# Performance work log

Measured on AMD Instinct MI355X. Metric: run time of the kernel, lower is better.

## Reference

```python
import jax, jax.numpy as jnp
import numpy as np

# ---- left-hand kinematic constants (from ShadowHandModule.create_left_hand_nodes_and_joints) ----
N_NODES = 29
PARENTS = [-1, 0, 1, 2, 3, 4, 5, 1, 7, 8, 9, 10, 1, 12, 13, 14, 15, 1, 17, 18, 19, 20, 21, 1, 23, 24, 25, 26, 27]
# joint index driving each node (-1 = fixed link such as fingertips)
NODE_JOINT = [0, 1, 2, 3, 4, 5, -1, 6, 7, 8, 9, -1, 10, 11, 12, 13, -1, 14, 15, 16, 17, 18, -1, 19, 20, 21, 22, 23, -1]
TRANS = np.array([
    [0.0, 0.0, 0.0], [0.0, 0.0, 0.034],
    [-0.033, 0.0, 0.095], [0.0, 0.0, 0.0], [0.0, 0.0, 0.045], [0.0, 0.0, 0.025], [0.0, 0.0, 0.026],
    [-0.011, 0.0, 0.099], [0.0, 0.0, 0.0], [0.0, 0.0, 0.045], [0.0, 0.0, 0.025], [0.0, 0.0, 0.026],
    [0.011, 0.0, 0.095], [0.0, 0.0, 0.0], [0.0, 0.0, 0.045], [0.0, 0.0, 0.025], [0.0, 0.0, 0.026],
    [0.033, 0.0, 0.02071], [0.0, 0.0, 0.06579], [0.0, 0.0, 0.0], [0.0, 0.0, 0.045], [0.0, 0.0, 0.025], [0.0, 0.0, 0.026],
    [-0.034, -0.0085, 0.029], [0.0, 0.0, 0.0], [0.0, 0.0, 0.038], [0.0, 0.0, 0.0], [0.0, 0.0, 0.032], [0.0, 0.0, 0.0275],
], dtype=np.float32)
AXES = np.array([
    [0.0, 1.0, 0.0], [1.0, 0.0, 0.0],
    [0.0, 1.0, 0.0], [1.0, 0.0, 0.0], [1.0, 0.0, 0.0], [1.0, 0.0, 0.0],
    [0.0, 1.0, 0.0], [1.0, 0.0, 0.0], [1.0, 0.0, 0.0], [1.0, 0.0, 0.0],
    [0.0, -1.0, 0.0], [1.0, 0.0, 0.0], [1.0, 0.0, 0.0], [1.0, 0.0, 0.0],
    [0.573576, 0.0, -0.819152], [0.0, -1.0, 0.0], [1.0, 0.0, 0.0], [1.0, 0.0, 0.0], [1.0, 0.0, 0.0],
    [0.0, 0.0, 1.0], [-1.0, 0.0, 0.0], [1.0, 0.0, 0.0], [0.0, -1.0, 0.0], [1.0, 0.0, 0.0],
], dtype=np.float32)
MIN_RAD = np.array([-0.523599, -0.698132, -0.349066, 0.0, 0.0, 0.0, -0.349066, 0.0, 0.0, 0.0,
                    -0.349066, 0.0, 0.0, 0.0, 0.0, -0.349066, 0.0, 0.0, 0.0,
                    -1.0472, 0.0, -0.20944, -0.698132, 0.0], dtype=np.float32)
MAX_RAD = np.array([0.174533, 0.488692, 0.349066, 1.5708, 1.5708, 1.5708, 0.349066, 1.5708, 1.5708, 1.5708,
                    0.349066, 1.5708, 1.5708, 1.5708, 0.785398, 0.349066, 1.5708, 1.5708, 1.5708,
                    1.0472, 1.22173, 0.20944, 0.698132, 1.5708], dtype=np.float32)
THBASE_QUAT = np.array([0.0, 0.382683, 0.0, -0.92388], dtype=np.float32)
THDISTAL_QUAT = np.array([0.707107, 0.0, 0.0, -0.707107], dtype=np.float32)
BATCH = 262144


def hat(v):
    x, y, z = v[..., 0], v[..., 1], v[..., 2]
    o = jnp.zeros_like(x)
    return jnp.stack([jnp.stack([o, -z, y], -1),
                      jnp.stack([z, o, -x], -1),
                      jnp.stack([-y, x, o], -1)], -2)


def rot_angle_axis(angle, axis):
    # angle [B,J], axis [J,3] -> [B,J,3,3] (Rodrigues)
    s = jnp.sin(angle)[..., None, None]
    c = jnp.cos(angle)[..., None, None]
    K = hat(axis)          # [J,3,3]
    K2 = jnp.matmul(K, K)  # [J,3,3]
    return jnp.eye(3, dtype=angle.dtype) + s * K + (1.0 - c) * K2


def rot_from_quat(q):
    w, x, y, z = q[0], q[1], q[2], q[3]
    return jnp.array([
        [1.0 - 2.0 * (y * y + z * z), 2.0 * (x * y - z * w), 2.0 * (x * z + y * w)],
        [2.0 * (x * y + z * w), 1.0 - 2.0 * (x * x + z * z), 2.0 * (y * z - x * w)],
        [2.0 * (x * z - y * w), 2.0 * (y * z + x * w), 1.0 - 2.0 * (x * x + y * y)],
    ], dtype=q.dtype)


def setup_inputs() -> dict:
    key = jax.random.key(0)
    u = jax.random.uniform(key, (BATCH, 24), dtype=jnp.float32)
    angles = jnp.asarray(MIN_RAD) + u * jnp.asarray(MAX_RAD - MIN_RAD)
    return {"angles": angles}


def reference(angles):
    # angles: [B, 24] joint angles -> node positions [B, 29, 3]
    B = angles.shape[0]
    q = jnp.clip(angles, jnp.asarray(MIN_RAD), jnp.asarray(MAX_RAD))
    Rj = rot_angle_axis(q, jnp.asarray(AXES))  # [B,24,3,3]
    fixed = {23: rot_from_quat(jnp.asarray(THBASE_QUAT)),
             27: rot_from_quat(jnp.asarray(THDISTAL_QUAT))}
    eye = jnp.broadcast_to(jnp.eye(3, dtype=angles.dtype), (B, 3, 3))
    Rg = [None] * N_NODES
    tg = [None] * N_NODES
    for i in range(N_NODES):  # fixed 29-node kinematic tree, topological order
        j = NODE_JOINT[i]
        Rl = Rj[:, j] if j >= 0 else eye
        if i in fixed:  # body quat applied before joint rotation (MJCF convention)
            Rl = jnp.einsum('ij,bjk->bik', fixed[i], Rl)
        tl = jnp.asarray(TRANS[i])
        p = PARENTS[i]
        if p < 0:
            Rg[i] = Rl
            tg[i] = jnp.broadcast_to(tl, (B, 3))
        else:
            # multiply_transform: (Rp @ Rl, Rp @ tl + tp)
            Rg[i] = jnp.einsum('bij,bjk->bik', Rg[p], Rl)
            tg[i] = jnp.einsum('bij,j->bi', Rg[p], tl) + tg[p]
    return jnp.stack(tg, axis=1)  # [B, 29, 3]
```

## Files before the change

kernel.cpp:

```cpp
#include <hip/hip_runtime.h>

namespace fk {

typedef float f32x4 __attribute__((ext_vector_type(4)));

struct V3 { float x, y, z; };
struct M3 { V3 c0, c1, c2; };

__device__ __forceinline__ V3 axpy(float a, V3 x, V3 y) {
    return V3{ fmaf(a, x.x, y.x), fmaf(a, x.y, y.y), fmaf(a, x.z, y.z) };
}
__device__ __forceinline__ V3 sc(float a, V3 x) { return V3{ a * x.x, a * x.y, a * x.z }; }

__device__ __forceinline__ M3 mulRx(const M3& R, float s, float c) {
    return M3{ R.c0,
               axpy(s,  R.c2, sc(c, R.c1)),
               axpy(-s, R.c1, sc(c, R.c2)) };
}
__device__ __forceinline__ M3 mulRy(const M3& R, float s, float c) {
    return M3{ axpy(-s, R.c2, sc(c, R.c0)),
               R.c1,
               axpy(s,  R.c0, sc(c, R.c2)) };
}

__global__ __launch_bounds__(64) void fk_kernel(const float* __restrict__ angles,
                                                float* __restrict__ out, int B) {
    __shared__ float lds[64 * 87];

    const int tid = threadIdx.x;
    const int b = blockIdx.x * 64 + tid;
    const bool valid = (b < B);

    if (valid) {
        const float4* ap = reinterpret_cast<const float4*>(angles + (size_t)b * 24);
        float q[24];
        {
            float4 v;
            v = ap[0]; q[0]=v.x;  q[1]=v.y;  q[2]=v.z;  q[3]=v.w;
            v = ap[1]; q[4]=v.x;  q[5]=v.y;  q[6]=v.z;  q[7]=v.w;
            v = ap[2]; q[8]=v.x;  q[9]=v.y;  q[10]=v.z; q[11]=v.w;
            v = ap[3]; q[12]=v.x; q[13]=v.y; q[14]=v.z; q[15]=v.w;
            v = ap[4]; q[16]=v.x; q[17]=v.y; q[18]=v.z; q[19]=v.w;
            v = ap[5]; q[20]=v.x; q[21]=v.y; q[22]=v.z; q[23]=v.w;
        }

        constexpr float MN[24] = {-0.523599f,-0.698132f,-0.349066f,0.f,0.f,0.f,-0.349066f,0.f,0.f,0.f,
                                  -0.349066f,0.f,0.f,0.f,0.f,-0.349066f,0.f,0.f,0.f,
                                  -1.0472f,0.f,-0.20944f,-0.698132f,0.f};
        constexpr float MX[24] = {0.174533f,0.488692f,0.349066f,1.5708f,1.5708f,1.5708f,0.349066f,1.5708f,1.5708f,1.5708f,
                                  0.349066f,1.5708f,1.5708f,1.5708f,0.785398f,0.349066f,1.5708f,1.5708f,1.5708f,
                                  1.0472f,1.22173f,0.20944f,0.698132f,1.5708f};
        float s[24], c[24];
        #pragma unroll
        for (int j = 0; j < 24; ++j) {
            float a = fminf(fmaxf(q[j], MN[j]), MX[j]);
            __sincosf(a, &s[j], &c[j]);
        }

        float* o = lds + tid * 87;
        auto emit = [&](int node, V3 t) {
            o[node*3+0] = t.x; o[node*3+1] = t.y; o[node*3+2] = t.z;
        };

        M3 R0{ V3{c[0],0.f,-s[0]}, V3{0.f,1.f,0.f}, V3{s[0],0.f,c[0]} };
        emit(0, V3{0.f,0.f,0.f});
        M3 R1 = mulRx(R0, s[1], c[1]);
        V3 t1 = sc(0.034f, R0.c2);
        emit(1, t1);

        auto finger = [&](int n0, float sy, float cy,
                          float s1, float c1, float s2, float c2, float s3, float c3,
                          float bx, float bz) {
            M3 Ra = mulRy(R1, sy, cy);
            V3 ta = axpy(bx, R1.c0, axpy(bz, R1.c2, t1));
            emit(n0, ta);
            M3 Rb = mulRx(Ra, s1, c1);
            emit(n0+1, ta);
            V3 tc = axpy(0.045f, Rb.c2, ta);
            M3 Rc = mulRx(Rb, s2, c2);
            emit(n0+2, tc);
            V3 td = axpy(0.025f, Rc.c2, tc);
            M3 Rd = mulRx(Rc, s3, c3);
            emit(n0+3, td);
            emit(n0+4, axpy(0.026f, Rd.c2, td));
        };
        finger(2,   s[2],  c[2],  s[3],c[3],   s[4],c[4],   s[5],c[5],  -0.033f, 0.095f);
        finger(7,   s[6],  c[6],  s[7],c[7],   s[8],c[8],   s[9],c[9],  -0.011f, 0.099f);
        finger(12, -s[10], c[10], s[11],c[11], s[12],c[12], s[13],c[13], 0.011f, 0.095f);

        {
            const float ux = 0.573576f, uz = -0.819152f;
            float omc = 1.f - c[14];
            float l00 = fmaf(omc * ux, ux, c[14]);
            float l10 = s[14] * uz;
            float l20 = omc * ux * uz;
            float l01 = -s[14] * uz;
            float l21 = s[14] * ux;
            float l02 = omc * ux * uz;
            float l12 = -s[14] * ux;
            float l22 = fmaf(omc * uz, uz, c[14]);
            M3 R17;
            R17.c0 = axpy(l20, R1.c2, axpy(l10,  R1.c1, sc(l00, R1.c0)));
            R17.c1 = axpy(l21, R1.c2, axpy(c[14],R1.c1, sc(l01, R1.c0)));
            R17.c2 = axpy(l22, R1.c2, axpy(l12,  R1.c1, sc(l02, R1.c0)));
            V3 t17 = axpy(0.033f, R1.c0, axpy(0.02071f, R1.c2, t1));
            emit(17, t17);
            V3 t18 = axpy(0.06579f, R17.c2, t17);
            M3 R18 = mulRy(R17, -s[15], c[15]);
            emit(18, t18);
            M3 R19 = mulRx(R18, s[16], c[16]);
            emit(19, t18);
            V3 t20 = axpy(0.045f, R19.c2, t18);
            M3 R20 = mulRx(R19, s[17], c[17]);
            emit(20, t20);
            V3 t21 = axpy(0.025f, R20.c2, t20);
            M3 R21 = mulRx(R20, s[18], c[18]);
            emit(21, t21);
            emit(22, axpy(0.026f, R21.c2, t21));
        }

        {
            const float k = 0.70710678f;
            float m00 = -k * c[19], m10 = -s[19];
            float m01 =  k * s[19], m11 = -c[19];
            M3 R23;
            R23.c0 = axpy(m00, R1.c2, axpy(m10, R1.c1, sc(m00, R1.c0)));
            R23.c1 = axpy(m01, R1.c2, axpy(m11, R1.c1, sc(m01, R1.c0)));
            R23.c2 = axpy(k, R1.c2, sc(-k, R1.c0));
            V3 t23 = axpy(-0.034f, R1.c0, axpy(-0.0085f, R1.c1, axpy(0.029f, R1.c2, t1)));
            emit(23, t23);
            M3 R24 = mulRx(R23, -s[20], c[20]);
            emit(24, t23);
            V3 t25 = axpy(0.038f, R24.c2, t23);
            M3 R25 = mulRx(R24, s[21], c[21]);
            emit(25, t25);
            M3 R26 = mulRy(R25, -s[22], c[22]);
            emit(26, t25);
            V3 t27 = axpy(0.032f, R26.c2, t25);
            M3 R27;
            R27.c0 = sc(-1.f, R26.c1);
            R27.c1 = axpy(s[23],  R26.c2, sc(c[23], R26.c0));
            R27.c2 = axpy(-s[23], R26.c0, sc(c[23], R26.c2));
            emit(27, t27);
            emit(28, axpy(0.0275f, R27.c2, t27));
        }
    }

    __syncthreads();

    const size_t base_f = (size_t)blockIdx.x * 64 * 87;
    if ((size_t)(blockIdx.x + 1) * 64 <= (size_t)B) {
        const f32x4* lsrc = reinterpret_cast<const f32x4*>(lds);
        f32x4* gdst = reinterpret_cast<f32x4*>(out + base_f);
        #pragma unroll
        for (int m = 0; m < 21; ++m)
            __builtin_nontemporal_store(lsrc[m * 64 + tid], &gdst[m * 64 + tid]);
        int g = 21 * 64 + tid;
        if (g < 1392) __builtin_nontemporal_store(lsrc[g], &gdst[g]);
    } else {
        const size_t limit = (size_t)B * 87;
        for (int m = 0; m < 87; ++m) {
            size_t f = (size_t)m * 64 + tid;
            if (base_f + f < limit) __builtin_nontemporal_store(lds[f], &out[base_f + f]);
        }
    }
}

}

extern "C" void kernel_launch(void* const* d_in, const int* in_sizes, int n_in,
                              void* d_out, int out_size, void* d_ws, size_t ws_size,
                              hipStream_t stream) {
    const float* angles = (const float*)d_in[0];
    float* out = (float*)d_out;
    const int B = in_sizes[0] / 24;
    const int grid = (B + 63) / 64;
    fk::fk_kernel<<<grid, 64, 0, stream>>>(angles, out, B);
}
```

Baseline: 23.06 us.

## Use a capped grid where each block loops over slabs and prefetches the next angles

The grid is capped at 1024 single-wave blocks, and each block loops over K consecutive 64-element slabs instead of handling one. Inside the loop, the next slab's angles are loaded while the current slab is computed and flushed. The aim is to overlap input loads with compute and output stores, and to cut block launch overhead. The costs are far fewer resident waves per CU for hiding memory latency, and removal of the __syncthreads. That removal relies on the 64-thread block being a single wavefront, so LDS writes and the cross-lane reads stay ordered.

```diff
diff --git a/kernel.cpp b/kernel.cpp
--- a/kernel.cpp
+++ b/kernel.cpp
@@ -23,133 +23,127 @@
                axpy(s,  R.c0, sc(c, R.c2)) };
 }
 
-__global__ __launch_bounds__(64) void fk_kernel(const float* __restrict__ angles,
-                                                float* __restrict__ out, int B) {
-    __shared__ float lds[64 * 87];
+__device__ __forceinline__ void load_angles(f32x4 v[6], const float* __restrict__ angles,
+                                            long long elem, int B) {
+    if (elem < B) {
+        const f32x4* ap = reinterpret_cast<const f32x4*>(angles + (size_t)elem * 24);
+        #pragma unroll
+        for (int m = 0; m < 6; ++m) v[m] = ap[m];
+    }
+}
 
-    const int tid = threadIdx.x;
-    const int b = blockIdx.x * 64 + tid;
-    const bool valid = (b < B);
-
-    if (valid) {
-        const float4* ap = reinterpret_cast<const float4*>(angles + (size_t)b * 24);
-        float q[24];
-        {
-            float4 v;
-            v = ap[0]; q[0]=v.x;  q[1]=v.y;  q[2]=v.z;  q[3]=v.w;
-            v = ap[1]; q[4]=v.x;  q[5]=v.y;  q[6]=v.z;  q[7]=v.w;
-            v = ap[2]; q[8]=v.x;  q[9]=v.y;  q[10]=v.z; q[11]=v.w;
-            v = ap[3]; q[12]=v.x; q[13]=v.y; q[14]=v.z; q[15]=v.w;
-            v = ap[4]; q[16]=v.x; q[17]=v.y; q[18]=v.z; q[19]=v.w;
-            v = ap[5]; q[20]=v.x; q[21]=v.y; q[22]=v.z; q[23]=v.w;
-        }
-
-        constexpr float MN[24] = {-0.523599f,-0.698132f,-0.349066f,0.f,0.f,0.f,-0.349066f,0.f,0.f,0.f,
-                                  -0.349066f,0.f,0.f,0.f,0.f,-0.349066f,0.f,0.f,0.f,
-                                  -1.0472f,0.f,-0.20944f,-0.698132f,0.f};
-        constexpr float MX[24] = {0.174533f,0.488692f,0.349066f,1.5708f,1.5708f,1.5708f,0.349066f,1.5708f,1.5708f,1.5708f,
-                                  0.349066f,1.5708f,1.5708f,1.5708f,0.785398f,0.349066f,1.5708f,1.5708f,1.5708f,
-                                  1.0472f,1.22173f,0.20944f,0.698132f,1.5708f};
-        float s[24], c[24];
-        #pragma unroll
-        for (int j = 0; j < 24; ++j) {
-            float a = fminf(fmaxf(q[j], MN[j]), MX[j]);
-            __sincosf(a, &s[j], &c[j]);
-        }
-
-        float* o = lds + tid * 87;
-        auto emit = [&](int node, V3 t) {
-            o[node*3+0] = t.x; o[node*3+1] = t.y; o[node*3+2] = t.z;
-        };
-
-        M3 R0{ V3{c[0],0.f,-s[0]}, V3{0.f,1.f,0.f}, V3{s[0],0.f,c[0]} };
-        emit(0, V3{0.f,0.f,0.f});
-        M3 R1 = mulRx(R0, s[1], c[1]);
-        V3 t1 = sc(0.034f, R0.c2);
-        emit(1, t1);
-
-        auto finger = [&](int n0, float sy, float cy,
-                          float s1, float c1, float s2, float c2, float s3, float c3,
-                          float bx, float bz) {
-            M3 Ra = mulRy(R1, sy, cy);
-            V3 ta = axpy(bx, R1.c0, axpy(bz, R1.c2, t1));
-            emit(n0, ta);
-            M3 Rb = mulRx(Ra, s1, c1);
-            emit(n0+1, ta);
-            V3 tc = axpy(0.045f, Rb.c2, ta);
-            M3 Rc = mulRx(Rb, s2, c2);
-            emit(n0+2, tc);
-            V3 td = axpy(0.025f, Rc.c2, tc);
-            M3 Rd = mulRx(Rc, s3, c3);
-            emit(n0+3, td);
-            emit(n0+4, axpy(0.026f, Rd.c2, td));
-        };
-        finger(2,   s[2],  c[2],  s[3],c[3],   s[4],c[4],   s[5],c[5],  -0.033f, 0.095f);
-        finger(7,   s[6],  c[6],  s[7],c[7],   s[8],c[8],   s[9],c[9],  -0.011f, 0.099f);
-        finger(12, -s[10], c[10], s[11],c[11], s[12],c[12], s[13],c[13], 0.011f, 0.095f);
-
-        {
-            const float ux = 0.573576f, uz = -0.819152f;
-            float omc = 1.f - c[14];
-            float l00 = fmaf(omc * ux, ux, c[14]);
-            float l10 = s[14] * uz;
-            float l20 = omc * ux * uz;
-            float l01 = -s[14] * uz;
-            float l21 = s[14] * ux;
-            float l02 = omc * ux * uz;
-            float l12 = -s[14] * ux;
-            float l22 = fmaf(omc * uz, uz, c[14]);
-            M3 R17;
-            R17.c0 = axpy(l20, R1.c2, axpy(l10,  R1.c1, sc(l00, R1.c0)));
-            R17.c1 = axpy(l21, R1.c2, axpy(c[14],R1.c1, sc(l01, R1.c0)));
-            R17.c2 = axpy(l22, R1.c2, axpy(l12,  R1.c1, sc(l02, R1.c0)));
-            V3 t17 = axpy(0.033f, R1.c0, axpy(0.02071f, R1.c2, t1));
-            emit(17, t17);
-            V3 t18 = axpy(0.06579f, R17.c2, t17);
-            M3 R18 = mulRy(R17, -s[15], c[15]);
-            emit(18, t18);
-            M3 R19 = mulRx(R18, s[16], c[16]);
-            emit(19, t18);
-            V3 t20 = axpy(0.045f, R19.c2, t18);
-            M3 R20 = mulRx(R19, s[17], c[17]);
-            emit(20, t20);
-            V3 t21 = axpy(0.025f, R20.c2, t20);
-            M3 R21 = mulRx(R20, s[18], c[18]);
-            emit(21, t21);
-            emit(22, axpy(0.026f, R21.c2, t21));
-        }
-
-        {
-            const float k = 0.70710678f;
-            float m00 = -k * c[19], m10 = -s[19];
-            float m01 =  k * s[19], m11 = -c[19];
-            M3 R23;
-            R23.c0 = axpy(m00, R1.c2, axpy(m10, R1.c1, sc(m00, R1.c0)));
-            R23.c1 = axpy(m01, R1.c2, axpy(m11, R1.c1, sc(m01, R1.c0)));
-            R23.c2 = axpy(k, R1.c2, sc(-k, R1.c0));
-            V3 t23 = axpy(-0.034f, R1.c0, axpy(-0.0085f, R1.c1, axpy(0.029f, R1.c2, t1)));
-            emit(23, t23);
-            M3 R24 = mulRx(R23, -s[20], c[20]);
-            emit(24, t23);
-            V3 t25 = axpy(0.038f, R24.c2, t23);
-            M3 R25 = mulRx(R24, s[21], c[21]);
-            emit(25, t25);
-            M3 R26 = mulRy(R25, -s[22], c[22]);
-            emit(26, t25);
-            V3 t27 = axpy(0.032f, R26.c2, t25);
-            M3 R27;
-            R27.c0 = sc(-1.f, R26.c1);
-            R27.c1 = axpy(s[23],  R26.c2, sc(c[23], R26.c0));
-            R27.c2 = axpy(-s[23], R26.c0, sc(c[23], R26.c2));
-            emit(27, t27);
-            emit(28, axpy(0.0275f, R27.c2, t27));
-        }
+__device__ __forceinline__ void compute_element(const f32x4 v[6], float* o) {
+    float q[24];
+    #pragma unroll
+    for (int m = 0; m < 6; ++m) {
+        q[m*4+0] = v[m].x; q[m*4+1] = v[m].y; q[m*4+2] = v[m].z; q[m*4+3] = v[m].w;
     }
 
-    __syncthreads();
+    constexpr float MN[24] = {-0.523599f,-0.698132f,-0.349066f,0.f,0.f,0.f,-0.349066f,0.f,0.f,0.f,
+                              -0.349066f,0.f,0.f,0.f,0.f,-0.349066f,0.f,0.f,0.f,
+                              -1.0472f,0.f,-0.20944f,-0.698132f,0.f};
+    constexpr float MX[24] = {0.174533f,0.488692f,0.349066f,1.5708f,1.5708f,1.5708f,0.349066f,1.5708f,1.5708f,1.5708f,
+                              0.349066f,1.5708f,1.5708f,1.5708f,0.785398f,0.349066f,1.5708f,1.5708f,1.5708f,
+                              1.0472f,1.22173f,0.20944f,0.698132f,1.5708f};
+    float s[24], c[24];
+    #pragma unroll
+    for (int j = 0; j < 24; ++j) {
+        float a = fminf(fmaxf(q[j], MN[j]), MX[j]);
+        __sincosf(a, &s[j], &c[j]);
+    }
 
-    const size_t base_f = (size_t)blockIdx.x * 64 * 87;
-    if ((size_t)(blockIdx.x + 1) * 64 <= (size_t)B) {
+    auto emit = [&](int node, V3 t) {
+        o[node*3+0] = t.x; o[node*3+1] = t.y; o[node*3+2] = t.z;
+    };
+
+    M3 R0{ V3{c[0],0.f,-s[0]}, V3{0.f,1.f,0.f}, V3{s[0],0.f,c[0]} };
+    emit(0, V3{0.f,0.f,0.f});
+    M3 R1 = mulRx(R0, s[1], c[1]);
+    V3 t1 = sc(0.034f, R0.c2);
+    emit(1, t1);
+
+    auto finger = [&](int n0, float sy, float cy,
+                      float s1, float c1, float s2, float c2, float s3, float c3,
+                      float bx, float bz) {
+        M3 Ra = mulRy(R1, sy, cy);
+        V3 ta = axpy(bx, R1.c0, axpy(bz, R1.c2, t1));
+        emit(n0, ta);
+        M3 Rb = mulRx(Ra, s1, c1);
+        emit(n0+1, ta);
+        V3 tc = axpy(0.045f, Rb.c2, ta);
+        M3 Rc = mulRx(Rb, s2, c2);
+        emit(n0+2, tc);
+        V3 td = axpy(0.025f, Rc.c2, tc);
+        M3 Rd = mulRx(Rc, s3, c3);
+        emit(n0+3, td);
+        emit(n0+4, axpy(0.026f, Rd.c2, td));
+    };
+    finger(2,   s[2],  c[2],  s[3],c[3],   s[4],c[4],   s[5],c[5],  -0.033f, 0.095f);
+    finger(7,   s[6],  c[6],  s[7],c[7],   s[8],c[8],   s[9],c[9],  -0.011f, 0.099f);
+    finger(12, -s[10], c[10], s[11],c[11], s[12],c[12], s[13],c[13], 0.011f, 0.095f);
+
+    {
+        const float ux = 0.573576f, uz = -0.819152f;
+        float omc = 1.f - c[14];
+        float l00 = fmaf(omc * ux, ux, c[14]);
+        float l10 = s[14] * uz;
+        float l20 = omc * ux * uz;
+        float l01 = -s[14] * uz;
+        float l21 = s[14] * ux;
+        float l02 = omc * ux * uz;
+        float l12 = -s[14] * ux;
+        float l22 = fmaf(omc * uz, uz, c[14]);
+        M3 R17;
+        R17.c0 = axpy(l20, R1.c2, axpy(l10,  R1.c1, sc(l00, R1.c0)));
+        R17.c1 = axpy(l21, R1.c2, axpy(c[14],R1.c1, sc(l01, R1.c0)));
+        R17.c2 = axpy(l22, R1.c2, axpy(l12,  R1.c1, sc(l02, R1.c0)));
+        V3 t17 = axpy(0.033f, R1.c0, axpy(0.02071f, R1.c2, t1));
+        emit(17, t17);
+        V3 t18 = axpy(0.06579f, R17.c2, t17);
+        M3 R18 = mulRy(R17, -s[15], c[15]);
+        emit(18, t18);
+        M3 R19 = mulRx(R18, s[16], c[16]);
+        emit(19, t18);
+        V3 t20 = axpy(0.045f, R19.c2, t18);
+        M3 R20 = mulRx(R19, s[17], c[17]);
+        emit(20, t20);
+        V3 t21 = axpy(0.025f, R20.c2, t20);
+        M3 R21 = mulRx(R20, s[18], c[18]);
+        emit(21, t21);
+        emit(22, axpy(0.026f, R21.c2, t21));
+    }
+
+    {
+        const float k = 0.70710678f;
+        float m00 = -k * c[19], m10 = -s[19];
+        float m01 =  k * s[19], m11 = -c[19];
+        M3 R23;
+        R23.c0 = axpy(m00, R1.c2, axpy(m10, R1.c1, sc(m00, R1.c0)));
+        R23.c1 = axpy(m01, R1.c2, axpy(m11, R1.c1, sc(m01, R1.c0)));
+        R23.c2 = axpy(k, R1.c2, sc(-k, R1.c0));
+        V3 t23 = axpy(-0.034f, R1.c0, axpy(-0.0085f, R1.c1, axpy(0.029f, R1.c2, t1)));
+        emit(23, t23);
+        M3 R24 = mulRx(R23, -s[20], c[20]);
+        emit(24, t23);
+        V3 t25 = axpy(0.038f, R24.c2, t23);
+        M3 R25 = mulRx(R24, s[21], c[21]);
+        emit(25, t25);
+        M3 R26 = mulRy(R25, -s[22], c[22]);
+        emit(26, t25);
+        V3 t27 = axpy(0.032f, R26.c2, t25);
+        M3 R27;
+        R27.c0 = sc(-1.f, R26.c1);
+        R27.c1 = axpy(s[23],  R26.c2, sc(c[23], R26.c0));
+        R27.c2 = axpy(-s[23], R26.c0, sc(c[23], R26.c2));
+        emit(27, t27);
+        emit(28, axpy(0.0275f, R27.c2, t27));
+    }
+}
+
+__device__ __forceinline__ void flush_slab(const float* lds, float* __restrict__ out,
+                                           long long s, int tid, int B) {
+    const size_t base_f = (size_t)s * 64 * 87;
+    if ((s + 1) * 64 <= (long long)B) {
         const f32x4* lsrc = reinterpret_cast<const f32x4*>(lds);
         f32x4* gdst = reinterpret_cast<f32x4*>(out + base_f);
         #pragma unroll
@@ -166,6 +160,27 @@
     }
 }
 
+__global__ __launch_bounds__(64) void fk_kernel(const float* __restrict__ angles,
+                                                float* __restrict__ out,
+                                                int B, int S, int K) {
+    __shared__ float lds[64 * 87];
+    const int tid = threadIdx.x;
+
+    long long s = (long long)blockIdx.x * K;
+    if (s >= S) return;
+    const long long s_end = min((long long)S, s + K);
+
+    f32x4 a6[6];
+    load_angles(a6, angles, s * 64 + tid, B);
+
+    for (; s < s_end; ++s) {
+        compute_element(a6, lds + tid * 87);
+        if (s + 1 < s_end)
+            load_angles(a6, angles, (s + 1) * 64 + tid, B);
+        flush_slab(lds, out, s, tid, B);
+    }
+}
+
 }
 
 extern "C" void kernel_launch(void* const* d_in, const int* in_sizes, int n_in,
@@ -174,6 +189,8 @@
     const float* angles = (const float*)d_in[0];
     float* out = (float*)d_out;
     const int B = in_sizes[0] / 24;
-    const int grid = (B + 63) / 64;
-    fk::fk_kernel<<<grid, 64, 0, stream>>>(angles, out, B);
+    const int S = (B + 63) / 64;
+    const int grid = S < 1024 ? S : 1024;
+    const int K = (S + grid - 1) / grid;
+    fk::fk_kernel<<<grid, 64, 0, stream>>>(angles, out, B, S, K);
 }
```

After: 24.25 us. 5.2% more time.
